# Kernel tuning notes

Hardware: AMD Instinct MI355X
Metric: run time of the kernel (lower is better)

## Reference

```python
import jax, jax.numpy as jnp
import numpy as np

DOT_THRESHOLD = 0.9995  # fall back to normalized lerp when quats nearly parallel
EPS = 1e-8


def _normalize(q, axis=-1):
    return q / jnp.clip(jnp.linalg.norm(q, axis=axis, keepdims=True), 1e-12)


def _quaternion_slerp(q0, q1, t):
    """Batched slerp. q0,q1: (N,4); t: (N,). Standard shortest-arc slerp."""
    dot = jnp.sum(q0 * q1, axis=-1)
    q1 = jnp.where(dot[..., None] < 0.0, -q1, q1)  # take shortest path
    dot = jnp.clip(jnp.abs(dot), -1.0, 1.0)
    theta = jnp.arccos(dot)
    sin_theta = jnp.sin(theta)
    safe_sin = jnp.where(sin_theta < EPS, 1.0, sin_theta)
    s0 = jnp.sin((1.0 - t) * theta) / safe_sin
    s1 = jnp.sin(t * theta) / safe_sin
    slerped = s0[..., None] * q0 + s1[..., None] * q1
    # near-parallel fallback: normalized linear interpolation
    lerped = _normalize(q0 + t[..., None] * (q1 - q0))
    return jnp.where(dot[..., None] > DOT_THRESHOLD, lerped, slerped)


def setup_inputs() -> dict:
    key = jax.random.key(0)
    k1, k2, k3 = jax.random.split(key, 3)
    N = 8_388_608  # number of time samples
    K = 64         # num_keyframes
    t = jax.random.uniform(k1, (N,), dtype=jnp.float32)
    translations = jax.random.normal(k2, (K, 3), dtype=jnp.float32) * 0.1
    quaternions = jax.random.normal(k3, (K, 4), dtype=jnp.float32)
    quaternions = quaternions.at[:, 0].add(2.0)  # bias toward identity like init
    keyframe_times = jnp.linspace(0.0, 1.0, K, dtype=jnp.float32)
    return {"t": t, "translations": translations, "quaternions": quaternions,
            "keyframe_times": keyframe_times}


def reference(t, translations, quaternions, keyframe_times):
    quats = _normalize(quaternions)  # F.normalize(self.quaternions, dim=-1)
    K = keyframe_times.shape[0]
    orig_shape = t.shape
    tf = t.reshape(-1)  # (N,)

    idx = jnp.searchsorted(keyframe_times, tf)  # left, matches torch default
    idx = jnp.clip(idx, 1, K - 1)
    idx_prev = idx - 1

    t_prev = keyframe_times[idx_prev]
    t_next = keyframe_times[idx]
    local_t = (tf - t_prev) / (t_next - t_prev + 1e-8)  # (N,)

    trans_prev = translations[idx_prev]  # (N,3)
    trans_next = translations[idx]
    quat_prev = quats[idx_prev]          # (N,4)
    quat_next = quats[idx]

    trans = (1.0 - local_t)[..., None] * trans_prev + local_t[..., None] * trans_next
    quat = _quaternion_slerp(quat_prev, quat_next, local_t)

    return trans.reshape(*orig_shape, 3), quat.reshape(*orig_shape, 4)
```

## Files before the change

### kernel.cpp

```cpp
#include <hip/hip_runtime.h>
#include <hip/hip_fp16.h>
#include <math.h>


#define KFR   64
#define NSEG  63
#define BLOCK 256
#define CHUNK 1024

typedef float v4f __attribute__((ext_vector_type(4)));

static __device__ __forceinline__ float pack2h(float a, float b) {
    __half2 h = __floats2half2_rn(a, b);
    unsigned int u;
    __builtin_memcpy(&u, &h, 4);
    return __uint_as_float(u);
}
static __device__ __forceinline__ float2 unpack2h(float p) {
    unsigned int u = __float_as_uint(p);
    __half2 h;
    __builtin_memcpy(&h, &u, 4);
    return __half22float2(h);
}

__global__ __launch_bounds__(BLOCK) void temporal_motor_kernel(
    const float* __restrict__ t_in,
    const float* __restrict__ translations,
    const float* __restrict__ quaternions,
    const float* __restrict__ keyframe_times,
    float* __restrict__ out_trans,
    float* __restrict__ out_quat,
    int nchunks)
{
    __shared__ float4 sA[KFR];
    __shared__ float4 sT[KFR];
    __shared__ float4 sQ[KFR];
    __shared__ __align__(16) float sStage[BLOCK / 64][192];

    const int tid = threadIdx.x;
    if (tid < NSEG) {
        const int s = tid;
        float t0 = keyframe_times[s];
        float t1 = keyframe_times[s + 1];

        float ax = quaternions[4 * s + 0], ay = quaternions[4 * s + 1];
        float az = quaternions[4 * s + 2], aw = quaternions[4 * s + 3];
        float bx = quaternions[4 * s + 4], by = quaternions[4 * s + 5];
        float bz = quaternions[4 * s + 6], bw = quaternions[4 * s + 7];
        float ia = 1.0f / fmaxf(sqrtf(ax * ax + ay * ay + az * az + aw * aw), 1e-12f);
        float ib = 1.0f / fmaxf(sqrtf(bx * bx + by * by + bz * bz + bw * bw), 1e-12f);
        ax *= ia; ay *= ia; az *= ia; aw *= ia;
        bx *= ib; by *= ib; bz *= ib; bw *= ib;

        float d0 = ax * bx + ay * by + az * bz + aw * bw;
        float sgn = (d0 < 0.0f) ? -1.0f : 1.0f;
        bx *= sgn; by *= sgn; bz *= sgn; bw *= sgn;
        float d = fminf(fabsf(d0), 1.0f);

        float theta  = acosf(d);
        float st     = sqrtf(fmaxf(1.0f - d * d, 0.0f));
        float inv_st = (d > 0.9995f) ? 0.0f : (1.0f / st);

        float px = translations[3 * s + 0], py = translations[3 * s + 1];
        float pz = translations[3 * s + 2];
        float dx = translations[3 * s + 3] - px;
        float dy = translations[3 * s + 4] - py;
        float dz = translations[3 * s + 5] - pz;

        sA[s] = make_float4(t0, t1, 1.0f / (t1 - t0 + 1e-8f), pack2h(theta, 1.0f - d));
        sT[s] = make_float4(pack2h(px, py), pack2h(pz, dx), pack2h(dy, dz), inv_st);
        sQ[s] = make_float4(pack2h(ax, ay), pack2h(az, aw), pack2h(bx, by), pack2h(bz, bw));
    }
    __syncthreads();

    const int lane = tid & 63;
    const int wave = tid >> 6;
    float* stg = sStage[wave];

    for (int chunk = blockIdx.x; chunk < nchunks; chunk += gridDim.x) {
        const int base = chunk * CHUNK + wave * 256 + lane;

        #pragma unroll
        for (int j = 0; j < 4; ++j) {
            const int idx = base + j * 64;
            const float tt = __builtin_nontemporal_load(t_in + idx);

            int s = (int)ceilf(tt * (float)NSEG) - 1;
            s = (s < 0) ? 0 : (s > NSEG - 1) ? NSEG - 1 : s;
            float4 a = sA[s];
            while (s > 0 && a.x >= tt)        { --s; a = sA[s]; }
            while (s < NSEG - 1 && a.y < tt)  { ++s; a = sA[s]; }

            const float lt  = (tt - a.x) * a.z;
            const float omt = 1.0f - lt;
            const float2 thd = unpack2h(a.w);

            const float4 tv   = sT[s];
            const float2 pxy  = unpack2h(tv.x);
            const float2 pzdx = unpack2h(tv.y);
            const float2 dydz = unpack2h(tv.z);
            const float inv_st = tv.w;

            float sn, cs;
            __sincosf(lt * thd.x, &sn, &cs);
            const float wbs = sn * inv_st;
            const float was = fmaf(thd.y, wbs, cs - wbs);

            const float s2  = fmaf(-2.0f * lt * omt, thd.y, 1.0f);
            const float inv = rsqrtf(fmaxf(s2, 1e-24f));
            const bool  fb  = (inv_st == 0.0f);
            const float wa  = fb ? omt * inv : was;
            const float wb  = fb ? lt * inv  : wbs;

            const float4 qv  = sQ[s];
            const float2 q0a = unpack2h(qv.x), q0b = unpack2h(qv.y);
            const float2 q1a = unpack2h(qv.z), q1b = unpack2h(qv.w);
            v4f oq;
            oq.x = wa * q0a.x + wb * q1a.x;
            oq.y = wa * q0a.y + wb * q1a.y;
            oq.z = wa * q0b.x + wb * q1b.x;
            oq.w = wa * q0b.y + wb * q1b.y;

            stg[lane * 3 + 0] = fmaf(lt, pzdx.y, pxy.x);
            stg[lane * 3 + 1] = fmaf(lt, dydz.x, pxy.y);
            stg[lane * 3 + 2] = fmaf(lt, dydz.y, pzdx.x);

            __builtin_nontemporal_store(oq, (v4f*)out_quat + idx);

            const int g = idx - lane;
            if (lane < 48) {
                v4f v = ((v4f*)stg)[lane];
                __builtin_nontemporal_store(v, (v4f*)(out_trans + (size_t)g * 3) + lane);
            }
        }
    }
}

__global__ void temporal_motor_tail(
    const float* __restrict__ t_in,
    const float* __restrict__ translations,
    const float* __restrict__ quaternions,
    const float* __restrict__ keyframe_times,
    float* __restrict__ out_trans,
    float* __restrict__ out_quat,
    int n_start, int n, int K)
{
    int i = n_start + blockIdx.x * blockDim.x + threadIdx.x;
    if (i >= n) return;
    float tt = t_in[i];

    int g = 1;
    while (g < K - 1 && keyframe_times[g] < tt) ++g;
    float tpw = keyframe_times[g - 1], tnw = keyframe_times[g];
    float lt = (tt - tpw) / (tnw - tpw + 1e-8f);
    float omt = 1.0f - lt;

    for (int c = 0; c < 3; ++c)
        out_trans[3 * (size_t)i + c] =
            omt * translations[3 * (g - 1) + c] + lt * translations[3 * g + c];

    float q0[4], q1[4];
    float n0 = 0, n1 = 0;
    for (int c = 0; c < 4; ++c) { q0[c] = quaternions[4 * (g - 1) + c]; n0 += q0[c] * q0[c]; }
    for (int c = 0; c < 4; ++c) { q1[c] = quaternions[4 * g + c];       n1 += q1[c] * q1[c]; }
    float i0 = 1.0f / fmaxf(sqrtf(n0), 1e-12f), i1 = 1.0f / fmaxf(sqrtf(n1), 1e-12f);
    float d = 0;
    for (int c = 0; c < 4; ++c) { q0[c] *= i0; q1[c] *= i1; }
    for (int c = 0; c < 4; ++c) d += q0[c] * q1[c];
    float sgn = (d < 0.0f) ? -1.0f : 1.0f;
    for (int c = 0; c < 4; ++c) q1[c] *= sgn;
    d = fminf(fabsf(d), 1.0f);
    float theta = acosf(d);
    float st = sqrtf(fmaxf(1.0f - d * d, 0.0f));
    float invst = (st < 1e-8f) ? 1.0f : (1.0f / st);
    float s0 = __sinf(omt * theta) * invst, s1 = __sinf(lt * theta) * invst;
    float l[4], ln = 0;
    for (int c = 0; c < 4; ++c) { l[c] = q0[c] + lt * (q1[c] - q0[c]); ln += l[c] * l[c]; }
    float li = 1.0f / fmaxf(sqrtf(ln), 1e-12f);
    bool fb = (d > 0.9995f);
    for (int c = 0; c < 4; ++c)
        out_quat[4 * (size_t)i + c] = fb ? l[c] * li : (s0 * q0[c] + s1 * q1[c]);
}

extern "C" void kernel_launch(void* const* d_in, const int* in_sizes, int n_in,
                              void* d_out, int out_size, void* d_ws, size_t ws_size,
                              hipStream_t stream) {
    const float* t_in  = (const float*)d_in[0];
    const float* trans = (const float*)d_in[1];
    const float* quats = (const float*)d_in[2];
    const float* ktime = (const float*)d_in[3];
    const int N = in_sizes[0];
    const int K = in_sizes[3];

    float* out_trans = (float*)d_out;
    float* out_quat  = (float*)d_out + (size_t)N * 3;

    if (K == KFR && (N & 3) == 0) {
        const int nchunks = N / CHUNK;
        if (nchunks > 0) {
            int blocks = nchunks < 2048 ? nchunks : 2048;
            temporal_motor_kernel<<<blocks, BLOCK, 0, stream>>>(
                t_in, trans, quats, ktime, out_trans, out_quat, nchunks);
        }
        const int rem_start = nchunks * CHUNK;
        if (rem_start < N) {
            int rem = N - rem_start;
            temporal_motor_tail<<<(rem + 63) / 64, 64, 0, stream>>>(
                t_in, trans, quats, ktime, out_trans, out_quat, rem_start, N, K);
        }
    } else {
        temporal_motor_tail<<<(N + 255) / 256, 256, 0, stream>>>(
            t_in, trans, quats, ktime, out_trans, out_quat, 0, N, K);
    }
}
```

Before: 266.2 us.

## Batch t loads per thread and store translations directly as vec3

```diff
diff --git a/kernel.cpp b/kernel.cpp
--- a/kernel.cpp
+++ b/kernel.cpp
@@ -6,9 +6,11 @@
 #define KFR   64
 #define NSEG  63
 #define BLOCK 256
-#define CHUNK 1024
+#define EPT   8
+#define CHUNK (BLOCK * EPT)
 
 typedef float v4f __attribute__((ext_vector_type(4)));
+typedef float v3f __attribute__((ext_vector_type(3)));
 
 static __device__ __forceinline__ float pack2h(float a, float b) {
     __half2 h = __floats2half2_rn(a, b);
@@ -35,7 +37,6 @@
     __shared__ float4 sA[KFR];
     __shared__ float4 sT[KFR];
     __shared__ float4 sQ[KFR];
-    __shared__ __align__(16) float sStage[BLOCK / 64][192];
 
     const int tid = threadIdx.x;
     if (tid < NSEG) {
@@ -75,23 +76,27 @@
 
     const int lane = tid & 63;
     const int wave = tid >> 6;
-    float* stg = sStage[wave];
 
     for (int chunk = blockIdx.x; chunk < nchunks; chunk += gridDim.x) {
-        const int base = chunk * CHUNK + wave * 256 + lane;
-
+        const int base = chunk * CHUNK + wave * (EPT * 64) + lane;
+
+        float tt[EPT];
         #pragma unroll
-        for (int j = 0; j < 4; ++j) {
+        for (int j = 0; j < EPT; ++j)
+            tt[j] = t_in[base + j * 64];
+
+        #pragma unroll
+        for (int j = 0; j < EPT; ++j) {
             const int idx = base + j * 64;
-            const float tt = __builtin_nontemporal_load(t_in + idx);
-
-            int s = (int)ceilf(tt * (float)NSEG) - 1;
+            const float t = tt[j];
+
+            int s = (int)ceilf(t * (float)NSEG) - 1;
             s = (s < 0) ? 0 : (s > NSEG - 1) ? NSEG - 1 : s;
             float4 a = sA[s];
-            while (s > 0 && a.x >= tt)        { --s; a = sA[s]; }
-            while (s < NSEG - 1 && a.y < tt)  { ++s; a = sA[s]; }
-
-            const float lt  = (tt - a.x) * a.z;
+            while (s > 0 && a.x >= t)        { --s; a = sA[s]; }
+            while (s < NSEG - 1 && a.y < t)  { ++s; a = sA[s]; }
+
+            const float lt  = (t - a.x) * a.z;
             const float omt = 1.0f - lt;
             const float2 thd = unpack2h(a.w);
 
@@ -121,17 +126,13 @@
             oq.z = wa * q0b.x + wb * q1b.x;
             oq.w = wa * q0b.y + wb * q1b.y;
 
-            stg[lane * 3 + 0] = fmaf(lt, pzdx.y, pxy.x);
-            stg[lane * 3 + 1] = fmaf(lt, dydz.x, pxy.y);
-            stg[lane * 3 + 2] = fmaf(lt, dydz.y, pzdx.x);
+            v3f tr;
+            tr.x = fmaf(lt, pzdx.y, pxy.x);
+            tr.y = fmaf(lt, dydz.x, pxy.y);
+            tr.z = fmaf(lt, dydz.y, pzdx.x);
 
             __builtin_nontemporal_store(oq, (v4f*)out_quat + idx);
-
-            const int g = idx - lane;
-            if (lane < 48) {
-                v4f v = ((v4f*)stg)[lane];
-                __builtin_nontemporal_store(v, (v4f*)(out_trans + (size_t)g * 3) + lane);
-            }
+            __builtin_nontemporal_store(tr, (v3f*)(out_trans + (size_t)idx * 3));
         }
     }
 }
@@ -198,7 +199,7 @@
     if (K == KFR && (N & 3) == 0) {
         const int nchunks = N / CHUNK;
         if (nchunks > 0) {
-            int blocks = nchunks < 2048 ? nchunks : 2048;
+            int blocks = nchunks < 4096 ? nchunks : 4096;
             temporal_motor_kernel<<<blocks, BLOCK, 0, stream>>>(
                 t_in, trans, quats, ktime, out_trans, out_quat, nchunks);
         }
```

Measured after the change: 264.5 us. About the same (-0.6%).
